# Optimization experiments

Hardware: AMD Instinct MI355X
Metric: run time of the kernel (lower is better)

Reference implementation:

```python
import jax, jax.numpy as jnp
import numpy as np

N_NODES = 10000
N_EDGES = 160000
D = 512
HID = 512
N_LAYERS = 3
N_CLASSES = 10
N_GRAPHS = 64


def setup_inputs() -> dict:
    key = jax.random.key(0)
    ks = jax.random.split(key, 8)
    x = jax.random.normal(ks[0], (N_NODES, D), dtype=jnp.float32)
    edge_index = jax.random.randint(ks[1], (2, N_EDGES), 0, N_NODES, dtype=jnp.int64)
    batch = jnp.sort(jax.random.randint(ks[2], (N_NODES,), 0, N_GRAPHS, dtype=jnp.int64))
    # GCNConv weights (in == hid == 512 for all layers, so stack them)
    scale_w = 1.0 / np.sqrt(HID)
    Ws = jax.random.normal(ks[3], (N_LAYERS, HID, HID), dtype=jnp.float32) * scale_w
    bs = jnp.zeros((N_LAYERS, HID), dtype=jnp.float32)
    lin_w = jax.random.normal(ks[4], (HID, N_CLASSES), dtype=jnp.float32) * scale_w
    lin_b = jnp.zeros((N_CLASSES,), dtype=jnp.float32)
    return {"x": x, "edge_index": edge_index, "batch": batch,
            "Ws": Ws, "bs": bs, "lin_w": lin_w, "lin_b": lin_b}


def reference(x, edge_index, batch, Ws, bs, lin_w, lin_b):
    N = x.shape[0]
    # GCNConv: add self-loops, symmetric deg^-1/2 normalization (computed once,
    # since the graph is fixed across layers)
    loops = jnp.arange(N, dtype=edge_index.dtype)
    row = jnp.concatenate([edge_index[0], loops])  # source
    col = jnp.concatenate([edge_index[1], loops])  # target (aggregation index)
    deg = jax.ops.segment_sum(jnp.ones_like(col, dtype=x.dtype), col, num_segments=N)
    dinv = jax.lax.rsqrt(deg)  # deg >= 1 thanks to self-loops
    norm = (dinv[row] * dinv[col])[:, None]  # [E+N, 1]

    for i in range(Ws.shape[0]):
        h = x @ Ws[i]                                   # [N, HID] dense transform
        out = jax.ops.segment_sum(h[row] * norm, col, num_segments=N)
        x = jax.nn.relu(out + bs[i])
        # dropout(p=0.5) is identity in eval mode

    pooled = jax.ops.segment_sum(x, batch, num_segments=N_GRAPHS)  # [G, HID]
    logits = pooled @ lin_w + lin_b                                 # [G, C]
    return jax.nn.log_softmax(logits, axis=1)
```

## Files before the change

### kernel.cpp

```cpp
#include <hip/hip_runtime.h>

#define N_NODES 10000
#define HID 512
#define MPAD 10112
#define N_GRAPHS 64
#define N_CLASSES 10

typedef __bf16 bf16_t;
typedef __bf16 bf16x8 __attribute__((ext_vector_type(8)));
typedef float  f32x4  __attribute__((ext_vector_type(4)));

__device__ __forceinline__ void gload16(const bf16_t* g, bf16_t* l) {
    __builtin_amdgcn_global_load_lds(
        (const __attribute__((address_space(1))) void*)g,
        (__attribute__((address_space(3))) void*)l,
        16, 0, 0);
}

__global__ void zero_k(int* __restrict__ cnt, int* __restrict__ cur,
                       bf16_t* __restrict__ xh_pad, float* __restrict__ pooled) {
    int i = blockIdx.x * 256 + threadIdx.x;
    if (i < N_NODES) { cnt[i] = 0; cur[i] = 0; }
    const int PCH = (MPAD - N_NODES) * HID / 8;
    uint4 z = {0, 0, 0, 0};
    if (i < PCH) *(uint4*)&xh_pad[i * 8] = z;
    if (i < N_GRAPHS * HID / 4) *(uint4*)&pooled[i * 4] = z;
}

#define CVX_B 2500
#define TRW_B 192
__global__ void setup_k(const float* __restrict__ x,
                        bf16_t* __restrict__ xh,
                        const float* __restrict__ W, bf16_t* __restrict__ whT,
                        const int* __restrict__ ecol, int* __restrict__ cnt, int E) {
    __shared__ float tile[64][65];
    int b = blockIdx.x, t = threadIdx.x;
    if (b < CVX_B) {
        int idx = (b * 256 + t) * 8;
        f32x4 v0 = *(const f32x4*)&x[idx];
        f32x4 v1 = *(const f32x4*)&x[idx + 4];
        float v[8] = {v0[0], v0[1], v0[2], v0[3], v1[0], v1[1], v1[2], v1[3]};
        bf16x8 hi;
#pragma unroll
        for (int j = 0; j < 8; ++j) hi[j] = (bf16_t)v[j];
        *(bf16x8*)&xh[idx] = hi;
    } else if (b < CVX_B + TRW_B) {
        int tt  = b - CVX_B;
        int lyr = tt >> 6;
        int rem = tt & 63;
        int k0  = (rem >> 3) * 64;
        int j0  = (rem & 7) * 64;
        const float* Wl = W + ((size_t)lyr << 18);
        int r = t >> 6, c = t & 63;
#pragma unroll
        for (int i = 0; i < 16; ++i) {
            int row = r + i * 4;
            tile[row][c] = Wl[(size_t)(k0 + row) * 512 + j0 + c];
        }
        __syncthreads();
        bf16_t* Ol = whT + ((size_t)lyr << 18);
#pragma unroll
        for (int i = 0; i < 16; ++i) {
            int row = r + i * 4;
            Ol[(size_t)(j0 + row) * 512 + k0 + c] = (bf16_t)tile[c][row];
        }
    } else {
        int e = (b - CVX_B - TRW_B) * 256 + t;
        if (e < E) atomicAdd(&cnt[ecol[e]], 1);
    }
}

__global__ __launch_bounds__(1024) void scan_k(const int* __restrict__ cnt,
                                               int* __restrict__ off,
                                               float* __restrict__ dinv) {
    __shared__ int s[1024];
    int t = threadIdx.x;
    int base = t * 10;
    int loc[10];
    int sum = 0;
#pragma unroll
    for (int j = 0; j < 10; ++j) {
        int n = base + j;
        int v = (n < N_NODES) ? cnt[n] : 0;
        if (n < N_NODES) dinv[n] = rsqrtf(1.0f + (float)v);
        loc[j] = sum;
        sum += v;
    }
    s[t] = sum;
    __syncthreads();
    for (int o = 1; o < 1024; o <<= 1) {
        int v = (t >= o) ? s[t - o] : 0;
        __syncthreads();
        s[t] += v;
        __syncthreads();
    }
    int pre = (t > 0) ? s[t - 1] : 0;
#pragma unroll
    for (int j = 0; j < 10; ++j) {
        int n = base + j;
        if (n <= N_NODES) off[n] = pre + loc[j];
    }
}

__global__ void scatter_k(const int* __restrict__ row, const int* __restrict__ col,
                          const int* __restrict__ off, int* __restrict__ cursor,
                          const float* __restrict__ dinv,
                          int2* __restrict__ epk, int E) {
    int e = blockIdx.x * 256 + threadIdx.x;
    if (e >= E) return;
    int c = col[e], r = row[e];
    int p = off[c] + atomicAdd(&cursor[c], 1);
    float w = dinv[r] * dinv[c];
    epk[p] = make_int2(r, __float_as_int(w));
}

__global__ __launch_bounds__(256) void gemm3(
    const bf16_t* __restrict__ xh,
    const bf16_t* __restrict__ wh,
    bf16_t* __restrict__ hh)
{
    __shared__ alignas(16) bf16_t sAh[2][64 * 32];
    __shared__ alignas(16) bf16_t sBh[2][128 * 32];

    const int t  = threadIdx.x;
    const int l  = t & 63;
    const int wv = t >> 6;
    const int wr = wv >> 1;
    const int wc = wv & 1;
    const int n0 = blockIdx.x * 128;
    const int m0 = blockIdx.y * 64;

    f32x4 acc[2][4];
#pragma unroll
    for (int m = 0; m < 2; ++m)
#pragma unroll
        for (int n = 0; n < 4; ++n) acc[m][n] = (f32x4){0.f, 0.f, 0.f, 0.f};

    const int lr  = l & 15;
    const int kgr = (l >> 4) * 8;
    const int srow = t >> 2;
    const int sce  = (t & 3) * 8;

    auto stage = [&](int buf, int kk) {
        size_t gA  = (size_t)(m0 + srow) * HID + kk + sce;
        size_t gB0 = (size_t)(n0 + srow) * HID + kk + sce;
        size_t gB1 = (size_t)(n0 + 64 + srow) * HID + kk + sce;
        gload16(&xh[gA],  &sAh[buf][t * 8]);
        gload16(&wh[gB0], &sBh[buf][t * 8]);
        gload16(&wh[gB1], &sBh[buf][(t + 256) * 8]);
    };

    stage(0, 0);
    __syncthreads();

    int cur = 0;
    for (int kk = 0; kk < HID; kk += 32) {
        if (kk + 32 < HID) stage(cur ^ 1, kk + 32);

        bf16x8 ah[2], bh[4];
#pragma unroll
        for (int m = 0; m < 2; ++m) {
            int row = wr * 32 + m * 16 + lr;
            ah[m] = *(const bf16x8*)&sAh[cur][row * 32 + kgr];
        }
#pragma unroll
        for (int n = 0; n < 4; ++n) {
            int col = wc * 64 + n * 16 + lr;
            bh[n] = *(const bf16x8*)&sBh[cur][col * 32 + kgr];
        }
#pragma unroll
        for (int m = 0; m < 2; ++m)
#pragma unroll
            for (int n = 0; n < 4; ++n)
                acc[m][n] = __builtin_amdgcn_mfma_f32_16x16x32_bf16(ah[m], bh[n], acc[m][n], 0, 0, 0);

        __syncthreads();
        cur ^= 1;
    }

    const int rq = (l >> 4) * 4;
#pragma unroll
    for (int m = 0; m < 2; ++m) {
        int row = m0 + wr * 32 + m * 16 + rq;
#pragma unroll
        for (int n = 0; n < 4; ++n) {
            int col = n0 + wc * 64 + n * 16 + lr;
#pragma unroll
            for (int r = 0; r < 4; ++r)
                hh[(size_t)(row + r) * HID + col] = (bf16_t)acc[m][n][r];
        }
    }
}

template <bool LAST>
__global__ __launch_bounds__(256) void agg_k(
    const bf16_t* __restrict__ hh, const int* __restrict__ off,
    const int2* __restrict__ epk,
    const float* __restrict__ dinv, const float* __restrict__ bias,
    bf16_t* __restrict__ xh, float* __restrict__ x3)
{
    int node = blockIdx.x * 4 + (threadIdx.x >> 6);
    if (node >= N_NODES) return;
    int l  = threadIdx.x & 63;
    int c0 = l * 8;

    float dn = dinv[node];
    float sw = dn * dn;
    float a[8];
    {
        bf16x8 sv = *(const bf16x8*)&hh[(size_t)node * HID + c0];
#pragma unroll
        for (int j = 0; j < 8; ++j) a[j] = (float)sv[j] * sw;
    }

    int e0 = off[node], e1 = off[node + 1];
    int e = e0;
    for (; e + 4 <= e1; e += 4) {
        int4 p0 = *(const int4*)&epk[e];
        int4 p1 = *(const int4*)&epk[e + 2];
        bf16x8 v0 = *(const bf16x8*)&hh[(size_t)p0.x * HID + c0];
        bf16x8 v1 = *(const bf16x8*)&hh[(size_t)p0.z * HID + c0];
        bf16x8 v2 = *(const bf16x8*)&hh[(size_t)p1.x * HID + c0];
        bf16x8 v3 = *(const bf16x8*)&hh[(size_t)p1.z * HID + c0];
        float w0 = __int_as_float(p0.y), w1 = __int_as_float(p0.w);
        float w2 = __int_as_float(p1.y), w3 = __int_as_float(p1.w);
#pragma unroll
        for (int j = 0; j < 8; ++j) {
            a[j] += (float)v0[j] * w0 + (float)v1[j] * w1
                  + (float)v2[j] * w2 + (float)v3[j] * w3;
        }
    }
    for (; e < e1; ++e) {
        int2 ed = epk[e];
        float w = __int_as_float(ed.y);
        bf16x8 v = *(const bf16x8*)&hh[(size_t)ed.x * HID + c0];
#pragma unroll
        for (int j = 0; j < 8; ++j) a[j] += (float)v[j] * w;
    }
#pragma unroll
    for (int j = 0; j < 8; ++j) {
        a[j] += bias[c0 + j];
        if (a[j] < 0.f) a[j] = 0.f;
    }

    if (LAST) {
        f32x4 o0 = {a[0], a[1], a[2], a[3]};
        f32x4 o1 = {a[4], a[5], a[6], a[7]};
        *(f32x4*)&x3[(size_t)node * HID + c0]     = o0;
        *(f32x4*)&x3[(size_t)node * HID + c0 + 4] = o1;
    } else {
        bf16x8 hi;
#pragma unroll
        for (int j = 0; j < 8; ++j) hi[j] = (bf16_t)a[j];
        *(bf16x8*)&xh[(size_t)node * HID + c0] = hi;
    }
}

__global__ void pool_k(const float* __restrict__ x3, const int* __restrict__ batch,
                       float* __restrict__ pooled) {
    int t  = threadIdx.x;
    int n0 = blockIdx.x * 20;
    int nend = min(n0 + 20, N_NODES);
    float acc0 = 0.f, acc1 = 0.f;
    int cur = -1;
    for (int n = n0; n < nend; ++n) {
        int g = batch[n];
        if (g != cur) {
            if (cur >= 0) {
                atomicAdd(&pooled[cur * HID + t], acc0);
                atomicAdd(&pooled[cur * HID + t + 256], acc1);
            }
            cur = g; acc0 = 0.f; acc1 = 0.f;
        }
        acc0 += x3[(size_t)n * HID + t];
        acc1 += x3[(size_t)n * HID + t + 256];
    }
    if (cur >= 0) {
        atomicAdd(&pooled[cur * HID + t], acc0);
        atomicAdd(&pooled[cur * HID + t + 256], acc1);
    }
}

__global__ __launch_bounds__(64) void head_k(const float* __restrict__ pooled,
                                             const float* __restrict__ lw,
                                             const float* __restrict__ lb,
                                             float* __restrict__ out) {
    int g = blockIdx.x, l = threadIdx.x;
    float lg[10];
#pragma unroll
    for (int c = 0; c < N_CLASSES; ++c) {
        float s = 0.f;
        for (int k = l; k < HID; k += 64) s += pooled[g * HID + k] * lw[k * N_CLASSES + c];
        for (int o2 = 32; o2 > 0; o2 >>= 1) s += __shfl_down(s, o2);
        lg[c] = s;
    }
    if (l == 0) {
        float mx = -1e30f;
#pragma unroll
        for (int c = 0; c < N_CLASSES; ++c) { lg[c] += lb[c]; mx = fmaxf(mx, lg[c]); }
        float se = 0.f;
#pragma unroll
        for (int c = 0; c < N_CLASSES; ++c) se += expf(lg[c] - mx);
        float lse = logf(se);
#pragma unroll
        for (int c = 0; c < N_CLASSES; ++c) out[g * N_CLASSES + c] = lg[c] - mx - lse;
    }
}

extern "C" void kernel_launch(void* const* d_in, const int* in_sizes, int n_in,
                              void* d_out, int out_size, void* d_ws, size_t ws_size,
                              hipStream_t stream) {
    const float* x     = (const float*)d_in[0];
    const int*   ei    = (const int*)d_in[1];
    const int*   batch = (const int*)d_in[2];
    const float* Ws    = (const float*)d_in[3];
    const float* bs    = (const float*)d_in[4];
    const float* lw    = (const float*)d_in[5];
    const float* lb    = (const float*)d_in[6];
    float*       out   = (float*)d_out;
    const int E = in_sizes[1] / 2;
    const int* erow = ei;
    const int* ecol = ei + E;

    char* p = (char*)d_ws;
    auto take = [&](size_t bytes) {
        char* q = p;
        p += (bytes + 255) & ~(size_t)255;
        return q;
    };
    bf16_t* xh    = (bf16_t*)take((size_t)MPAD * HID * 2);
    bf16_t* hh    = (bf16_t*)take((size_t)MPAD * HID * 2);
    float*  x3    = (float*) take((size_t)N_NODES * HID * 4);
    bf16_t* whT   = (bf16_t*)take((size_t)3 * HID * HID * 2);
    float*  dinv  = (float*) take((size_t)N_NODES * 4);
    int*    cnt   = (int*)   take((size_t)N_NODES * 4);
    int*    off   = (int*)   take((size_t)(N_NODES + 1) * 4);
    int*    cur   = (int*)   take((size_t)N_NODES * 4);
    int2*   epk   = (int2*)  take((size_t)E * 8 + 64);
    float*  pooled= (float*) take((size_t)N_GRAPHS * HID * 4);

    const int cdeg_b = (E + 255) / 256;
    zero_k<<<40, 256, 0, stream>>>(cnt, cur, xh + (size_t)N_NODES * HID, pooled);
    setup_k<<<CVX_B + TRW_B + cdeg_b, 256, 0, stream>>>(
        x, xh, Ws, whT, ecol, cnt, E);
    scan_k<<<1, 1024, 0, stream>>>(cnt, off, dinv);
    scatter_k<<<cdeg_b, 256, 0, stream>>>(erow, ecol, off, cur, dinv, epk, E);

    for (int lyr = 0; lyr < 3; ++lyr) {
        gemm3<<<dim3(4, 158), 256, 0, stream>>>(
            xh, whT + (size_t)lyr * HID * HID, hh);
        if (lyr < 2)
            agg_k<false><<<(N_NODES + 3) / 4, 256, 0, stream>>>(
                hh, off, epk, dinv, bs + lyr * HID, xh, nullptr);
        else
            agg_k<true><<<(N_NODES + 3) / 4, 256, 0, stream>>>(
                hh, off, epk, dinv, bs + lyr * HID, nullptr, x3);
    }
    pool_k<<<500, 256, 0, stream>>>(x3, batch, pooled);
    head_k<<<N_GRAPHS, 64, 0, stream>>>(pooled, lw, lb, out);
}
```

Measured before the change: 179.3 us.

## Split each node's edge list across two waves and fuse pooling into last aggregation

Each node's neighbor list is now split between two wavefronts, whose partial sums are combined through shared memory, so twice as many waves gather edges in parallel. The last layer's aggregation now adds ReLU outputs straight into the pooled buffer with atomics. This removes the fp32 x3 intermediate and the separate pool kernel. In exchange it adds a block barrier, half-idle waves in the epilogue, and one atomic per element per node contending on only 64 graph rows.

New measurement: 334.2 us. +86.3%, slower.

```diff
diff --git a/kernel.cpp b/kernel.cpp
--- a/kernel.cpp
+++ b/kernel.cpp
@@ -197,25 +197,35 @@
     const bf16_t* __restrict__ hh, const int* __restrict__ off,
     const int2* __restrict__ epk,
     const float* __restrict__ dinv, const float* __restrict__ bias,
-    bf16_t* __restrict__ xh, float* __restrict__ x3)
+    const int* __restrict__ batch,
+    bf16_t* __restrict__ xh, float* __restrict__ pooled)
 {
-    int node = blockIdx.x * 4 + (threadIdx.x >> 6);
-    if (node >= N_NODES) return;
+    __shared__ float red[2][HID];
+    int slot = threadIdx.x >> 7;
+    int w    = (threadIdx.x >> 6) & 1;
+    int node = blockIdx.x * 2 + slot;
     int l  = threadIdx.x & 63;
     int c0 = l * 8;
 
-    float dn = dinv[node];
-    float sw = dn * dn;
     float a[8];
-    {
+    int e0 = off[node], e1 = off[node + 1];
+    int mid = (e0 + e1 + 1) >> 1;
+    int es = w ? mid : e0;
+    int ee = w ? e1 : mid;
+
+    if (w == 0) {
+        float dn = dinv[node];
+        float sw = dn * dn;
         bf16x8 sv = *(const bf16x8*)&hh[(size_t)node * HID + c0];
 #pragma unroll
         for (int j = 0; j < 8; ++j) a[j] = (float)sv[j] * sw;
-    }
-
-    int e0 = off[node], e1 = off[node + 1];
-    int e = e0;
-    for (; e + 4 <= e1; e += 4) {
+    } else {
+#pragma unroll
+        for (int j = 0; j < 8; ++j) a[j] = 0.f;
+    }
+
+    int e = es;
+    for (; e + 4 <= ee; e += 4) {
         int4 p0 = *(const int4*)&epk[e];
         int4 p1 = *(const int4*)&epk[e + 2];
         bf16x8 v0 = *(const bf16x8*)&hh[(size_t)p0.x * HID + c0];
@@ -230,54 +240,36 @@
                   + (float)v2[j] * w2 + (float)v3[j] * w3;
         }
     }
-    for (; e < e1; ++e) {
+    for (; e < ee; ++e) {
         int2 ed = epk[e];
-        float w = __int_as_float(ed.y);
+        float ww = __int_as_float(ed.y);
         bf16x8 v = *(const bf16x8*)&hh[(size_t)ed.x * HID + c0];
 #pragma unroll
-        for (int j = 0; j < 8; ++j) a[j] += (float)v[j] * w;
-    }
-#pragma unroll
-    for (int j = 0; j < 8; ++j) {
-        a[j] += bias[c0 + j];
-        if (a[j] < 0.f) a[j] = 0.f;
-    }
-
-    if (LAST) {
-        f32x4 o0 = {a[0], a[1], a[2], a[3]};
-        f32x4 o1 = {a[4], a[5], a[6], a[7]};
-        *(f32x4*)&x3[(size_t)node * HID + c0]     = o0;
-        *(f32x4*)&x3[(size_t)node * HID + c0 + 4] = o1;
-    } else {
-        bf16x8 hi;
-#pragma unroll
-        for (int j = 0; j < 8; ++j) hi[j] = (bf16_t)a[j];
-        *(bf16x8*)&xh[(size_t)node * HID + c0] = hi;
-    }
-}
-
-__global__ void pool_k(const float* __restrict__ x3, const int* __restrict__ batch,
-                       float* __restrict__ pooled) {
-    int t  = threadIdx.x;
-    int n0 = blockIdx.x * 20;
-    int nend = min(n0 + 20, N_NODES);
-    float acc0 = 0.f, acc1 = 0.f;
-    int cur = -1;
-    for (int n = n0; n < nend; ++n) {
-        int g = batch[n];
-        if (g != cur) {
-            if (cur >= 0) {
-                atomicAdd(&pooled[cur * HID + t], acc0);
-                atomicAdd(&pooled[cur * HID + t + 256], acc1);
-            }
-            cur = g; acc0 = 0.f; acc1 = 0.f;
-        }
-        acc0 += x3[(size_t)n * HID + t];
-        acc1 += x3[(size_t)n * HID + t + 256];
-    }
-    if (cur >= 0) {
-        atomicAdd(&pooled[cur * HID + t], acc0);
-        atomicAdd(&pooled[cur * HID + t + 256], acc1);
+        for (int j = 0; j < 8; ++j) a[j] += (float)v[j] * ww;
+    }
+
+    if (w == 1) {
+#pragma unroll
+        for (int j = 0; j < 8; ++j) red[slot][c0 + j] = a[j];
+    }
+    __syncthreads();
+    if (w == 0) {
+#pragma unroll
+        for (int j = 0; j < 8; ++j) {
+            a[j] += red[slot][c0 + j] + bias[c0 + j];
+            if (a[j] < 0.f) a[j] = 0.f;
+        }
+        if (LAST) {
+            int g = batch[node];
+#pragma unroll
+            for (int j = 0; j < 8; ++j)
+                atomicAdd(&pooled[g * HID + c0 + j], a[j]);
+        } else {
+            bf16x8 hi;
+#pragma unroll
+            for (int j = 0; j < 8; ++j) hi[j] = (bf16_t)a[j];
+            *(bf16x8*)&xh[(size_t)node * HID + c0] = hi;
+        }
     }
 }
 
@@ -330,7 +322,6 @@
     };
     bf16_t* xh    = (bf16_t*)take((size_t)MPAD * HID * 2);
     bf16_t* hh    = (bf16_t*)take((size_t)MPAD * HID * 2);
-    float*  x3    = (float*) take((size_t)N_NODES * HID * 4);
     bf16_t* whT   = (bf16_t*)take((size_t)3 * HID * HID * 2);
     float*  dinv  = (float*) take((size_t)N_NODES * 4);
     int*    cnt   = (int*)   take((size_t)N_NODES * 4);
@@ -350,12 +341,11 @@
         gemm3<<<dim3(4, 158), 256, 0, stream>>>(
             xh, whT + (size_t)lyr * HID * HID, hh);
         if (lyr < 2)
-            agg_k<false><<<(N_NODES + 3) / 4, 256, 0, stream>>>(
-                hh, off, epk, dinv, bs + lyr * HID, xh, nullptr);
+            agg_k<false><<<N_NODES / 2, 256, 0, stream>>>(
+                hh, off, epk, dinv, bs + lyr * HID, batch, xh, nullptr);
         else
-            agg_k<true><<<(N_NODES + 3) / 4, 256, 0, stream>>>(
-                hh, off, epk, dinv, bs + lyr * HID, nullptr, x3);
-    }
-    pool_k<<<500, 256, 0, stream>>>(x3, batch, pooled);
+            agg_k<true><<<N_NODES / 2, 256, 0, stream>>>(
+                hh, off, epk, dinv, bs + lyr * HID, batch, nullptr, pooled);
+    }
     head_k<<<N_GRAPHS, 64, 0, stream>>>(pooled, lw, lb, out);
 }
```
